# Performance work log

Measured on AMD Instinct MI355X. Metric: run time of the kernel, lower is better.

Reference implementation:

```python
import jax, jax.numpy as jnp
import numpy as np

B, T, U, D = 2, 512, 48, 512
H, K = 1024, 128  # hidden_channels, num_classes; fc1 in = 2*D = 1024


def setup_inputs() -> dict:
    key = jax.random.key(0)
    ks = jax.random.split(key, 9)
    s = 0.02
    return {
        "img_feature": jax.random.normal(ks[0], (B, T, D), jnp.float32),
        "label_feature": jax.random.normal(ks[1], (B, U, D), jnp.float32),
        "masks": jnp.ones((B, 1, T), jnp.float32),
        "W1": jax.random.normal(ks[2], (H, 2 * D), jnp.float32) * s,
        "b1": jnp.zeros((H,), jnp.float32),
        "W2": jax.random.normal(ks[3], (K, H), jnp.float32) * s,
        "b2": jnp.zeros((K,), jnp.float32),
        "conv_w": jax.random.normal(ks[4], (K, D), jnp.float32) * s,
        "conv_b": jnp.zeros((K,), jnp.float32),
    }


def reference(img_feature, label_feature, masks, W1, b1, W2, b2, conv_w, conv_b):
    # pointwise Conv1d over img features: (B,T,D) -> (B,K,T), masked
    img_seg_score = (jnp.einsum('btd,kd->bkt', img_feature, conv_w)
                     + conv_b[None, :, None]) * masks
    # fc1(cat(label, img)) == label @ Wl^T + img @ Wi^T + b1 (broadcast add),
    # avoiding the O(B*U*T*2D) repeat+cat intermediate.
    d = label_feature.shape[-1]
    Wl, Wi = W1[:, :d], W1[:, d:]
    lab = jnp.einsum('bud,hd->buh', label_feature, Wl)  # (B,U,H)
    img = jnp.einsum('btd,hd->bth', img_feature, Wi)    # (B,T,H)
    h = jnp.tanh(lab[:, :, None, :] + img[:, None, :, :] + b1)  # (B,U,T,H)
    joint = jnp.einsum('buth,kh->butk', h, W2) + b2
    joint_score = jax.nn.log_softmax(joint, axis=-1)
    return (img_seg_score, joint_score)
```

## Files before the change

### kernel.cpp

```cpp
#include <hip/hip_runtime.h>
#include <math.h>

#define BB 2
#define TT 512
#define UU 48
#define DD 512
#define HH 1024
#define KK 128

typedef _Float16 f16x8 __attribute__((ext_vector_type(8)));
typedef __fp16 fp16x2_t __attribute__((ext_vector_type(2)));
typedef float floatx4 __attribute__((ext_vector_type(4)));

__device__ __forceinline__ f16x8 tanh8z(f16x8 z) {
    f16x8 o;
#pragma unroll
    for (int i = 0; i < 8; i += 2) {
        float e0 = __builtin_amdgcn_exp2f((float)z[i]);
        float e1 = __builtin_amdgcn_exp2f((float)z[i + 1]);
        float r0 = __builtin_amdgcn_rcpf(e0 + 1.0f);
        float r1 = __builtin_amdgcn_rcpf(e1 + 1.0f);
        fp16x2_t p = __builtin_amdgcn_cvt_pkrtz(fmaf(-2.0f, r0, 1.0f),
                                                fmaf(-2.0f, r1, 1.0f));
        o[i] = (_Float16)p[0];
        o[i + 1] = (_Float16)p[1];
    }
    return o;
}

__global__ __launch_bounds__(256) void mid_kernel5(
    const float* __restrict__ img, const float* __restrict__ labf,
    const float* __restrict__ W1, const float* __restrict__ W2,
    const float* __restrict__ conv_w,
    const float* __restrict__ b1, const float* __restrict__ conv_b,
    const float* __restrict__ masks,
    _Float16* __restrict__ imgHf, _Float16* __restrict__ labHf,
    _Float16* __restrict__ W2s, float* __restrict__ seg_out) {
    int bid = blockIdx.x, tid = threadIdx.x;
    if (bid >= 624) {
        int base = (bid - 624) * 256 + tid;
#pragma unroll
        for (int i = 0; i < 32; ++i) {
            int o = base + i * 4096;
            int hg = o >> 10, kk2 = (o >> 3) & 127, hl = o & 7;
            W2s[o] = (_Float16)W2[(size_t)kk2 * HH + hg * 8 + hl];
        }
        return;
    }
    __shared__ __align__(16) _Float16 a_s[32][72];
    __shared__ __align__(16) _Float16 w_s[4096];
    const float* Arow;
    const float* Wbase;
    int r0, n0b, wstride, region;
    if (bid < 512) {
        region = 0; Arow = img; Wbase = W1 + 512; wstride = 2 * DD;
        int xcd = bid & 7, j = bid >> 3;
        r0 = (j & 31) * 32; n0b = (xcd * 2 + (j >> 5)) * 64;
    } else if (bid < 560) {
        region = 1; Arow = labf; Wbase = W1; wstride = 2 * DD;
        int i = bid - 512; r0 = (i % 3) * 32; n0b = (i / 3) * 64;
    } else {
        region = 2; Arow = img; Wbase = conv_w; wstride = DD;
        int i = bid - 560; r0 = (i >> 1) * 32; n0b = (i & 1) * 64;
    }
    int lane = tid & 63, wv = tid >> 6;
    int m0 = (wv & 1) * 16, n0w = (wv >> 1) * 32;
    int q = lane >> 4, r = lane & 15;
    int arow = tid >> 3, acol = (tid & 7) * 8;
    int wn = tid >> 2, wk0 = (tid & 3) * 16;
    const float* aptr = &Arow[(size_t)(r0 + arow) * DD + acol];
    const float* wptr = &Wbase[(size_t)(n0b + wn) * wstride + wk0];
    floatx4 acc[2] = {};
    float4 pa0, pa1, pw[4];
    pa0 = *(const float4*)aptr;
    pa1 = *(const float4*)(aptr + 4);
#pragma unroll
    for (int i2 = 0; i2 < 4; ++i2) pw[i2] = *(const float4*)(wptr + i2 * 4);
    for (int c = 0; c < 8; ++c) {
        f16x8 av;
        av[0] = (_Float16)pa0.x; av[1] = (_Float16)pa0.y;
        av[2] = (_Float16)pa0.z; av[3] = (_Float16)pa0.w;
        av[4] = (_Float16)pa1.x; av[5] = (_Float16)pa1.y;
        av[6] = (_Float16)pa1.z; av[7] = (_Float16)pa1.w;
        *(f16x8*)&a_s[arow][acol] = av;
        f16x8 w0, w1;
        w0[0] = (_Float16)pw[0].x; w0[1] = (_Float16)pw[0].y;
        w0[2] = (_Float16)pw[0].z; w0[3] = (_Float16)pw[0].w;
        w0[4] = (_Float16)pw[1].x; w0[5] = (_Float16)pw[1].y;
        w0[6] = (_Float16)pw[1].z; w0[7] = (_Float16)pw[1].w;
        w1[0] = (_Float16)pw[2].x; w1[1] = (_Float16)pw[2].y;
        w1[2] = (_Float16)pw[2].z; w1[3] = (_Float16)pw[2].w;
        w1[4] = (_Float16)pw[3].x; w1[5] = (_Float16)pw[3].y;
        w1[6] = (_Float16)pw[3].z; w1[7] = (_Float16)pw[3].w;
        int kg = wk0 >> 3;
        *(f16x8*)&w_s[((kg + 0) * 64 + wn) * 8] = w0;
        *(f16x8*)&w_s[((kg + 1) * 64 + wn) * 8] = w1;
        __syncthreads();
        if (c < 7) {
            int cb = (c + 1) * 64;
            pa0 = *(const float4*)(aptr + cb);
            pa1 = *(const float4*)(aptr + cb + 4);
#pragma unroll
            for (int i2 = 0; i2 < 4; ++i2)
                pw[i2] = *(const float4*)(wptr + cb + i2 * 4);
        }
#pragma unroll
        for (int kt = 0; kt < 2; ++kt) {
            f16x8 af = *(const f16x8*)&a_s[m0 + r][kt * 32 + q * 8];
#pragma unroll
            for (int nt = 0; nt < 2; ++nt) {
                f16x8 bf = *(const f16x8*)
                    &w_s[((kt * 4 + q) * 64 + n0w + nt * 16 + r) * 8];
                acc[nt] = __builtin_amdgcn_mfma_f32_16x16x32_f16(
                    af, bf, acc[nt], 0, 0, 0);
            }
        }
        __syncthreads();
    }
    const float SC = 2.8853900817779268f;
    if (region == 0) {
#pragma unroll
        for (int nt = 0; nt < 2; ++nt) {
            int n = n0b + n0w + nt * 16 + r;
#pragma unroll
            for (int rr = 0; rr < 4; ++rr)
                imgHf[(size_t)(r0 + m0 + 4 * q + rr) * HH + n] =
                    (_Float16)(acc[nt][rr] * SC);
        }
    } else if (region == 1) {
#pragma unroll
        for (int nt = 0; nt < 2; ++nt) {
            int n = n0b + n0w + nt * 16 + r;
            float bv = b1[n];
#pragma unroll
            for (int rr = 0; rr < 4; ++rr)
                labHf[(size_t)(r0 + m0 + 4 * q + rr) * HH + n] =
                    (_Float16)((acc[nt][rr] + bv) * SC);
        }
    } else {
#pragma unroll
        for (int nt = 0; nt < 2; ++nt) {
            int k = n0b + n0w + nt * 16 + r;
            float bv = conv_b[k];
#pragma unroll
            for (int rr = 0; rr < 4; ++rr) {
                int row = r0 + m0 + 4 * q + rr;
                int b = row >> 9, t = row & 511;
                seg_out[((size_t)b * KK + k) * TT + t] =
                    (acc[nt][rr] + bv) * masks[row];
            }
        }
    }
}

__global__ __launch_bounds__(192, 2) void joint_kernel7(
    const _Float16* __restrict__ imgHf,
    const _Float16* __restrict__ labHf,
    const _Float16* __restrict__ W2s,
    const float* __restrict__ b2,
    float* __restrict__ out) {
    __shared__ __align__(16) _Float16 w_s[2][8192];
    int tid = threadIdx.x, bid = blockIdx.x;
    int lane = tid & 63, wv = tid >> 6;
    int q = lane >> 4, r = lane & 15;
    int g0 = bid * 96 + wv * 32;
    int gr0 = g0 + r, gr1 = g0 + 16 + r;
    int bu0 = gr0 >> 9, t0 = gr0 & 511;
    int bu1 = gr1 >> 9, t1 = gr1 & 511;
    const _Float16* ir0 = imgHf + (size_t)(((bu0 >= UU) ? TT : 0) + t0) * HH;
    const _Float16* ir1 = imgHf + (size_t)(((bu1 >= UU) ? TT : 0) + t1) * HH;
    const _Float16* lr0 = labHf + (size_t)bu0 * HH;
    const _Float16* lr1 = labHf + (size_t)bu1 * HH;
    int c0 = q * 8, c1 = 32 + q * 8;
    floatx4 acc0[8] = {}, acc1[8] = {};
#pragma unroll
    for (int j = 0; j < 5; ++j)
        *(f16x8*)&w_s[0][(tid + j * 192) * 8] =
            *(const f16x8*)&W2s[(tid + j * 192) * 8];
    if (tid < 64)
        *(f16x8*)&w_s[0][(tid + 960) * 8] = *(const f16x8*)&W2s[(tid + 960) * 8];
    f16x8 i0A = *(const f16x8*)&ir0[c0], i0B = *(const f16x8*)&ir0[c1];
    f16x8 i1A = *(const f16x8*)&ir1[c0], i1B = *(const f16x8*)&ir1[c1];
    f16x8 l0A = *(const f16x8*)&lr0[c0], l0B = *(const f16x8*)&lr0[c1];
    f16x8 l1A = *(const f16x8*)&lr1[c0], l1B = *(const f16x8*)&lr1[c1];
    __syncthreads();
    for (int c = 0; c < 16; ++c) {
        _Float16* wb = w_s[c & 1];
        f16x8 ni0A, ni0B, ni1A, ni1B, nl0A, nl0B, nl1A, nl1B;
        f16x8 nw0, nw1, nw2, nw3, nw4, nw5;
        if (c < 15) {
            int cb = (c + 1) * 64;
            ni0A = *(const f16x8*)&ir0[cb + c0];
            ni0B = *(const f16x8*)&ir0[cb + c1];
            ni1A = *(const f16x8*)&ir1[cb + c0];
            ni1B = *(const f16x8*)&ir1[cb + c1];
            nl0A = *(const f16x8*)&lr0[cb + c0];
            nl0B = *(const f16x8*)&lr0[cb + c1];
            nl1A = *(const f16x8*)&lr1[cb + c0];
            nl1B = *(const f16x8*)&lr1[cb + c1];
            const _Float16* wsrc = W2s + (size_t)(c + 1) * 8192;
            nw0 = *(const f16x8*)&wsrc[(tid + 0 * 192) * 8];
            nw1 = *(const f16x8*)&wsrc[(tid + 1 * 192) * 8];
            nw2 = *(const f16x8*)&wsrc[(tid + 2 * 192) * 8];
            nw3 = *(const f16x8*)&wsrc[(tid + 3 * 192) * 8];
            nw4 = *(const f16x8*)&wsrc[(tid + 4 * 192) * 8];
            if (tid < 64) nw5 = *(const f16x8*)&wsrc[(tid + 960) * 8];
        }
        f16x8 a0A = tanh8z(i0A + l0A);
        f16x8 a1A = tanh8z(i1A + l1A);
#pragma unroll
        for (int nt = 0; nt < 8; ++nt) {
            f16x8 bf = *(const f16x8*)&wb[(q * 128 + nt * 16 + r) * 8];
            acc0[nt] = __builtin_amdgcn_mfma_f32_16x16x32_f16(
                a0A, bf, acc0[nt], 0, 0, 0);
            acc1[nt] = __builtin_amdgcn_mfma_f32_16x16x32_f16(
                a1A, bf, acc1[nt], 0, 0, 0);
        }
        f16x8 a0B = tanh8z(i0B + l0B);
        f16x8 a1B = tanh8z(i1B + l1B);
#pragma unroll
        for (int nt = 0; nt < 8; ++nt) {
            f16x8 bf = *(const f16x8*)&wb[((4 + q) * 128 + nt * 16 + r) * 8];
            acc0[nt] = __builtin_amdgcn_mfma_f32_16x16x32_f16(
                a0B, bf, acc0[nt], 0, 0, 0);
            acc1[nt] = __builtin_amdgcn_mfma_f32_16x16x32_f16(
                a1B, bf, acc1[nt], 0, 0, 0);
        }
        if (c < 15) {
            _Float16* wn_ = w_s[(c & 1) ^ 1];
            *(f16x8*)&wn_[(tid + 0 * 192) * 8] = nw0;
            *(f16x8*)&wn_[(tid + 1 * 192) * 8] = nw1;
            *(f16x8*)&wn_[(tid + 2 * 192) * 8] = nw2;
            *(f16x8*)&wn_[(tid + 3 * 192) * 8] = nw3;
            *(f16x8*)&wn_[(tid + 4 * 192) * 8] = nw4;
            if (tid < 64) *(f16x8*)&wn_[(tid + 960) * 8] = nw5;
            i0A = ni0A; i0B = ni0B; i1A = ni1A; i1B = ni1B;
            l0A = nl0A; l0B = nl0B; l1A = nl1A; l1B = nl1B;
        }
        __syncthreads();
    }
    float b2v[8];
#pragma unroll
    for (int nt = 0; nt < 8; ++nt) b2v[nt] = b2[nt * 16 + r];
#pragma unroll
    for (int mt = 0; mt < 2; ++mt) {
        float* obase = out + (size_t)(g0 + mt * 16 + 4 * q) * KK;
#pragma unroll
        for (int rr = 0; rr < 4; ++rr) {
            float v[8];
            float mx = -INFINITY;
#pragma unroll
            for (int nt = 0; nt < 8; ++nt) {
                v[nt] = (mt ? acc1[nt][rr] : acc0[nt][rr]) + b2v[nt];
                mx = fmaxf(mx, v[nt]);
            }
            mx = fmaxf(mx, __shfl_xor(mx, 1, 16));
            mx = fmaxf(mx, __shfl_xor(mx, 2, 16));
            mx = fmaxf(mx, __shfl_xor(mx, 4, 16));
            mx = fmaxf(mx, __shfl_xor(mx, 8, 16));
            float s = 0.f;
#pragma unroll
            for (int nt = 0; nt < 8; ++nt) s += __expf(v[nt] - mx);
            s += __shfl_xor(s, 1, 16);
            s += __shfl_xor(s, 2, 16);
            s += __shfl_xor(s, 4, 16);
            s += __shfl_xor(s, 8, 16);
            float lse = mx + __logf(s);
#pragma unroll
            for (int nt = 0; nt < 8; ++nt)
                obase[(size_t)rr * KK + nt * 16 + r] = v[nt] - lse;
        }
    }
}

extern "C" void kernel_launch(void* const* d_in, const int* in_sizes, int n_in,
                              void* d_out, int out_size, void* d_ws, size_t ws_size,
                              hipStream_t stream) {
    const float* img    = (const float*)d_in[0];
    const float* labf   = (const float*)d_in[1];
    const float* masks  = (const float*)d_in[2];
    const float* W1     = (const float*)d_in[3];
    const float* b1     = (const float*)d_in[4];
    const float* W2     = (const float*)d_in[5];
    const float* b2     = (const float*)d_in[6];
    const float* conv_w = (const float*)d_in[7];
    const float* conv_b = (const float*)d_in[8];
    float* out = (float*)d_out;

    _Float16* base  = (_Float16*)d_ws;
    _Float16* imgHf = base;
    _Float16* labHf = imgHf + 1024 * 1024;
    _Float16* W2s   = labHf + 96 * 1024;

    mid_kernel5<<<640, 256, 0, stream>>>(img, labf, W1, W2, conv_w,
                                         b1, conv_b, masks,
                                         imgHf, labHf, W2s, out);
    joint_kernel7<<<512, 192, 0, stream>>>(imgHf, labHf, W2s, b2,
                                           out + (size_t)BB * KK * TT);
}
```

Measured before the change: 125.9 us.

## Split joint kernel H reduction across two wave groups with LDS reduction

The joint kernel now uses 384 threads per block: two groups of three waves each handle half of the hidden dimension (8 chunks instead of 16) for the same 96 output rows. Each group keeps its own double-buffered W2 slice in shared memory, which grows shared memory to four buffers. Partial accumulators are exchanged through LDS and summed, and each group then computes log-softmax for one of the two 16-row tiles. The aim is to halve the serial loop length per wave and raise the number of waves in flight, at the cost of more shared memory, an extra reduction pass and possibly lower block occupancy.

```diff
diff --git a/kernel.cpp b/kernel.cpp
--- a/kernel.cpp
+++ b/kernel.cpp
@@ -153,43 +153,52 @@
     }
 }
 
-__global__ __launch_bounds__(192, 2) void joint_kernel7(
+__global__ __launch_bounds__(384, 3) void joint_kernel8(
     const _Float16* __restrict__ imgHf,
     const _Float16* __restrict__ labHf,
     const _Float16* __restrict__ W2s,
     const float* __restrict__ b2,
     float* __restrict__ out) {
-    __shared__ __align__(16) _Float16 w_s[2][8192];
+    __shared__ __align__(16) _Float16 w_s[4][8192];
     int tid = threadIdx.x, bid = blockIdx.x;
-    int lane = tid & 63, wv = tid >> 6;
+    int wv = tid >> 6;
+    int grp = (wv >= 3) ? 1 : 0;
+    int p = grp ? wv - 3 : wv;
+    int lt = tid - grp * 192;
+    int lane = tid & 63;
     int q = lane >> 4, r = lane & 15;
-    int g0 = bid * 96 + wv * 32;
+    int g0 = bid * 96 + p * 32;
     int gr0 = g0 + r, gr1 = g0 + 16 + r;
     int bu0 = gr0 >> 9, t0 = gr0 & 511;
     int bu1 = gr1 >> 9, t1 = gr1 & 511;
-    const _Float16* ir0 = imgHf + (size_t)(((bu0 >= UU) ? TT : 0) + t0) * HH;
-    const _Float16* ir1 = imgHf + (size_t)(((bu1 >= UU) ? TT : 0) + t1) * HH;
-    const _Float16* lr0 = labHf + (size_t)bu0 * HH;
-    const _Float16* lr1 = labHf + (size_t)bu1 * HH;
+    const _Float16* ir0 =
+        imgHf + (size_t)(((bu0 >= UU) ? TT : 0) + t0) * HH + grp * 512;
+    const _Float16* ir1 =
+        imgHf + (size_t)(((bu1 >= UU) ? TT : 0) + t1) * HH + grp * 512;
+    const _Float16* lr0 = labHf + (size_t)bu0 * HH + grp * 512;
+    const _Float16* lr1 = labHf + (size_t)bu1 * HH + grp * 512;
+    const _Float16* wsrc0 = W2s + (size_t)grp * 8 * 8192;
     int c0 = q * 8, c1 = 32 + q * 8;
     floatx4 acc0[8] = {}, acc1[8] = {};
+    _Float16* wbuf0 = w_s[grp * 2 + 0];
+    _Float16* wbuf1 = w_s[grp * 2 + 1];
 #pragma unroll
     for (int j = 0; j < 5; ++j)
-        *(f16x8*)&w_s[0][(tid + j * 192) * 8] =
-            *(const f16x8*)&W2s[(tid + j * 192) * 8];
-    if (tid < 64)
-        *(f16x8*)&w_s[0][(tid + 960) * 8] = *(const f16x8*)&W2s[(tid + 960) * 8];
+        *(f16x8*)&wbuf0[(lt + j * 192) * 8] =
+            *(const f16x8*)&wsrc0[(lt + j * 192) * 8];
+    if (lt < 64)
+        *(f16x8*)&wbuf0[(lt + 960) * 8] = *(const f16x8*)&wsrc0[(lt + 960) * 8];
     f16x8 i0A = *(const f16x8*)&ir0[c0], i0B = *(const f16x8*)&ir0[c1];
     f16x8 i1A = *(const f16x8*)&ir1[c0], i1B = *(const f16x8*)&ir1[c1];
     f16x8 l0A = *(const f16x8*)&lr0[c0], l0B = *(const f16x8*)&lr0[c1];
     f16x8 l1A = *(const f16x8*)&lr1[c0], l1B = *(const f16x8*)&lr1[c1];
     __syncthreads();
-    for (int c = 0; c < 16; ++c) {
-        _Float16* wb = w_s[c & 1];
+    for (int s = 0; s < 8; ++s) {
+        _Float16* wb = (s & 1) ? wbuf1 : wbuf0;
         f16x8 ni0A, ni0B, ni1A, ni1B, nl0A, nl0B, nl1A, nl1B;
         f16x8 nw0, nw1, nw2, nw3, nw4, nw5;
-        if (c < 15) {
-            int cb = (c + 1) * 64;
+        if (s < 7) {
+            int cb = (s + 1) * 64;
             ni0A = *(const f16x8*)&ir0[cb + c0];
             ni0B = *(const f16x8*)&ir0[cb + c1];
             ni1A = *(const f16x8*)&ir1[cb + c0];
@@ -198,13 +207,13 @@
             nl0B = *(const f16x8*)&lr0[cb + c1];
             nl1A = *(const f16x8*)&lr1[cb + c0];
             nl1B = *(const f16x8*)&lr1[cb + c1];
-            const _Float16* wsrc = W2s + (size_t)(c + 1) * 8192;
-            nw0 = *(const f16x8*)&wsrc[(tid + 0 * 192) * 8];
-            nw1 = *(const f16x8*)&wsrc[(tid + 1 * 192) * 8];
-            nw2 = *(const f16x8*)&wsrc[(tid + 2 * 192) * 8];
-            nw3 = *(const f16x8*)&wsrc[(tid + 3 * 192) * 8];
-            nw4 = *(const f16x8*)&wsrc[(tid + 4 * 192) * 8];
-            if (tid < 64) nw5 = *(const f16x8*)&wsrc[(tid + 960) * 8];
+            const _Float16* wsrc = wsrc0 + (size_t)(s + 1) * 8192;
+            nw0 = *(const f16x8*)&wsrc[(lt + 0 * 192) * 8];
+            nw1 = *(const f16x8*)&wsrc[(lt + 1 * 192) * 8];
+            nw2 = *(const f16x8*)&wsrc[(lt + 2 * 192) * 8];
+            nw3 = *(const f16x8*)&wsrc[(lt + 3 * 192) * 8];
+            nw4 = *(const f16x8*)&wsrc[(lt + 4 * 192) * 8];
+            if (lt < 64) nw5 = *(const f16x8*)&wsrc[(lt + 960) * 8];
         }
         f16x8 a0A = tanh8z(i0A + l0A);
         f16x8 a1A = tanh8z(i1A + l1A);
@@ -226,50 +235,63 @@
             acc1[nt] = __builtin_amdgcn_mfma_f32_16x16x32_f16(
                 a1B, bf, acc1[nt], 0, 0, 0);
         }
-        if (c < 15) {
-            _Float16* wn_ = w_s[(c & 1) ^ 1];
-            *(f16x8*)&wn_[(tid + 0 * 192) * 8] = nw0;
-            *(f16x8*)&wn_[(tid + 1 * 192) * 8] = nw1;
-            *(f16x8*)&wn_[(tid + 2 * 192) * 8] = nw2;
-            *(f16x8*)&wn_[(tid + 3 * 192) * 8] = nw3;
-            *(f16x8*)&wn_[(tid + 4 * 192) * 8] = nw4;
-            if (tid < 64) *(f16x8*)&wn_[(tid + 960) * 8] = nw5;
+        if (s < 7) {
+            _Float16* wn_ = (s & 1) ? wbuf0 : wbuf1;
+            *(f16x8*)&wn_[(lt + 0 * 192) * 8] = nw0;
+            *(f16x8*)&wn_[(lt + 1 * 192) * 8] = nw1;
+            *(f16x8*)&wn_[(lt + 2 * 192) * 8] = nw2;
+            *(f16x8*)&wn_[(lt + 3 * 192) * 8] = nw3;
+            *(f16x8*)&wn_[(lt + 4 * 192) * 8] = nw4;
+            if (lt < 64) *(f16x8*)&wn_[(lt + 960) * 8] = nw5;
             i0A = ni0A; i0B = ni0B; i1A = ni1A; i1B = ni1B;
             l0A = nl0A; l0B = nl0B; l1A = nl1A; l1B = nl1B;
         }
         __syncthreads();
     }
+    float* red = (float*)w_s;
+    {
+        float* myout = red + (size_t)(p * 2 + grp) * 2048;
+#pragma unroll
+        for (int nt = 0; nt < 8; ++nt)
+            *(floatx4*)&myout[nt * 256 + lane * 4] = grp ? acc0[nt] : acc1[nt];
+    }
+    __syncthreads();
+    {
+        float* other = red + (size_t)(p * 2 + (grp ^ 1)) * 2048;
+#pragma unroll
+        for (int nt = 0; nt < 8; ++nt) {
+            floatx4 v = *(const floatx4*)&other[nt * 256 + lane * 4];
+            if (grp) acc1[nt] += v; else acc0[nt] += v;
+        }
+    }
     float b2v[8];
 #pragma unroll
     for (int nt = 0; nt < 8; ++nt) b2v[nt] = b2[nt * 16 + r];
-#pragma unroll
-    for (int mt = 0; mt < 2; ++mt) {
-        float* obase = out + (size_t)(g0 + mt * 16 + 4 * q) * KK;
-#pragma unroll
-        for (int rr = 0; rr < 4; ++rr) {
-            float v[8];
-            float mx = -INFINITY;
-#pragma unroll
-            for (int nt = 0; nt < 8; ++nt) {
-                v[nt] = (mt ? acc1[nt][rr] : acc0[nt][rr]) + b2v[nt];
-                mx = fmaxf(mx, v[nt]);
-            }
-            mx = fmaxf(mx, __shfl_xor(mx, 1, 16));
-            mx = fmaxf(mx, __shfl_xor(mx, 2, 16));
-            mx = fmaxf(mx, __shfl_xor(mx, 4, 16));
-            mx = fmaxf(mx, __shfl_xor(mx, 8, 16));
-            float s = 0.f;
-#pragma unroll
-            for (int nt = 0; nt < 8; ++nt) s += __expf(v[nt] - mx);
-            s += __shfl_xor(s, 1, 16);
-            s += __shfl_xor(s, 2, 16);
-            s += __shfl_xor(s, 4, 16);
-            s += __shfl_xor(s, 8, 16);
-            float lse = mx + __logf(s);
-#pragma unroll
-            for (int nt = 0; nt < 8; ++nt)
-                obase[(size_t)rr * KK + nt * 16 + r] = v[nt] - lse;
-        }
+    float* obase = out + (size_t)(g0 + grp * 16 + 4 * q) * KK;
+#pragma unroll
+    for (int rr = 0; rr < 4; ++rr) {
+        float v[8];
+        float mx = -INFINITY;
+#pragma unroll
+        for (int nt = 0; nt < 8; ++nt) {
+            v[nt] = (grp ? acc1[nt][rr] : acc0[nt][rr]) + b2v[nt];
+            mx = fmaxf(mx, v[nt]);
+        }
+        mx = fmaxf(mx, __shfl_xor(mx, 1, 16));
+        mx = fmaxf(mx, __shfl_xor(mx, 2, 16));
+        mx = fmaxf(mx, __shfl_xor(mx, 4, 16));
+        mx = fmaxf(mx, __shfl_xor(mx, 8, 16));
+        float s = 0.f;
+#pragma unroll
+        for (int nt = 0; nt < 8; ++nt) s += __expf(v[nt] - mx);
+        s += __shfl_xor(s, 1, 16);
+        s += __shfl_xor(s, 2, 16);
+        s += __shfl_xor(s, 4, 16);
+        s += __shfl_xor(s, 8, 16);
+        float lse = mx + __logf(s);
+#pragma unroll
+        for (int nt = 0; nt < 8; ++nt)
+            obase[(size_t)rr * KK + nt * 16 + r] = v[nt] - lse;
     }
 }
 
@@ -295,6 +317,6 @@
     mid_kernel5<<<640, 256, 0, stream>>>(img, labf, W1, W2, conv_w,
                                          b1, conv_b, masks,
                                          imgHf, labHf, W2s, out);
-    joint_kernel7<<<512, 192, 0, stream>>>(imgHf, labHf, W2s, b2,
+    joint_kernel8<<<512, 384, 0, stream>>>(imgHf, labHf, W2s, b2,
                                            out + (size_t)BB * KK * TT);
 }
```

After: 128.7 us. +2.2%, slower.

## Use larger joint blocks with 4-chunk W2 staging per barrier

Applied to the files above, without the earlier changes.

Doubles the joint kernel block to 6 waves (192 rows) and launches half as many blocks. Each shared-memory W2 stage now holds four 64-wide H chunks (64 KB per buffer, 128 KB double-buffered), so barriers drop from 16 to 3 per block and each W2 load is shared by more rows. The costs are higher LDS usage, which may limit occupancy to one block per CU despite the launch bound of 2, more registers for the staged W2 prefetch, and only 256 blocks in the grid.

```diff
diff --git a/kernel.cpp b/kernel.cpp
--- a/kernel.cpp
+++ b/kernel.cpp
@@ -153,17 +153,17 @@
     }
 }
 
-__global__ __launch_bounds__(192, 2) void joint_kernel7(
+__global__ __launch_bounds__(384, 2) void joint_kernel9(
     const _Float16* __restrict__ imgHf,
     const _Float16* __restrict__ labHf,
     const _Float16* __restrict__ W2s,
     const float* __restrict__ b2,
     float* __restrict__ out) {
-    __shared__ __align__(16) _Float16 w_s[2][8192];
+    __shared__ __align__(16) _Float16 w_s[2][32768];
     int tid = threadIdx.x, bid = blockIdx.x;
     int lane = tid & 63, wv = tid >> 6;
-    int q = lane >> 4, r = lane & 15;
-    int g0 = bid * 96 + wv * 32;
+    int ql = lane >> 4, r = lane & 15;
+    int g0 = bid * 192 + wv * 32;
     int gr0 = g0 + r, gr1 = g0 + 16 + r;
     int bu0 = gr0 >> 9, t0 = gr0 & 511;
     int bu1 = gr1 >> 9, t1 = gr1 & 511;
@@ -171,80 +171,89 @@
     const _Float16* ir1 = imgHf + (size_t)(((bu1 >= UU) ? TT : 0) + t1) * HH;
     const _Float16* lr0 = labHf + (size_t)bu0 * HH;
     const _Float16* lr1 = labHf + (size_t)bu1 * HH;
-    int c0 = q * 8, c1 = 32 + q * 8;
+    int c0 = ql * 8, c1 = 32 + ql * 8;
     floatx4 acc0[8] = {}, acc1[8] = {};
 #pragma unroll
-    for (int j = 0; j < 5; ++j)
-        *(f16x8*)&w_s[0][(tid + j * 192) * 8] =
-            *(const f16x8*)&W2s[(tid + j * 192) * 8];
-    if (tid < 64)
-        *(f16x8*)&w_s[0][(tid + 960) * 8] = *(const f16x8*)&W2s[(tid + 960) * 8];
+    for (int k2 = 0; k2 < 10; ++k2)
+        *(f16x8*)&w_s[0][(tid + k2 * 384) * 8] =
+            *(const f16x8*)&W2s[(tid + k2 * 384) * 8];
+    if (tid < 256)
+        *(f16x8*)&w_s[0][(tid + 3840) * 8] =
+            *(const f16x8*)&W2s[(tid + 3840) * 8];
     f16x8 i0A = *(const f16x8*)&ir0[c0], i0B = *(const f16x8*)&ir0[c1];
     f16x8 i1A = *(const f16x8*)&ir1[c0], i1B = *(const f16x8*)&ir1[c1];
     f16x8 l0A = *(const f16x8*)&lr0[c0], l0B = *(const f16x8*)&lr0[c1];
     f16x8 l1A = *(const f16x8*)&lr1[c0], l1B = *(const f16x8*)&lr1[c1];
     __syncthreads();
-    for (int c = 0; c < 16; ++c) {
-        _Float16* wb = w_s[c & 1];
-        f16x8 ni0A, ni0B, ni1A, ni1B, nl0A, nl0B, nl1A, nl1B;
-        f16x8 nw0, nw1, nw2, nw3, nw4, nw5;
-        if (c < 15) {
-            int cb = (c + 1) * 64;
-            ni0A = *(const f16x8*)&ir0[cb + c0];
-            ni0B = *(const f16x8*)&ir0[cb + c1];
-            ni1A = *(const f16x8*)&ir1[cb + c0];
-            ni1B = *(const f16x8*)&ir1[cb + c1];
-            nl0A = *(const f16x8*)&lr0[cb + c0];
-            nl0B = *(const f16x8*)&lr0[cb + c1];
-            nl1A = *(const f16x8*)&lr1[cb + c0];
-            nl1B = *(const f16x8*)&lr1[cb + c1];
-            const _Float16* wsrc = W2s + (size_t)(c + 1) * 8192;
-            nw0 = *(const f16x8*)&wsrc[(tid + 0 * 192) * 8];
-            nw1 = *(const f16x8*)&wsrc[(tid + 1 * 192) * 8];
-            nw2 = *(const f16x8*)&wsrc[(tid + 2 * 192) * 8];
-            nw3 = *(const f16x8*)&wsrc[(tid + 3 * 192) * 8];
-            nw4 = *(const f16x8*)&wsrc[(tid + 4 * 192) * 8];
-            if (tid < 64) nw5 = *(const f16x8*)&wsrc[(tid + 960) * 8];
-        }
-        f16x8 a0A = tanh8z(i0A + l0A);
-        f16x8 a1A = tanh8z(i1A + l1A);
-#pragma unroll
-        for (int nt = 0; nt < 8; ++nt) {
-            f16x8 bf = *(const f16x8*)&wb[(q * 128 + nt * 16 + r) * 8];
-            acc0[nt] = __builtin_amdgcn_mfma_f32_16x16x32_f16(
-                a0A, bf, acc0[nt], 0, 0, 0);
-            acc1[nt] = __builtin_amdgcn_mfma_f32_16x16x32_f16(
-                a1A, bf, acc1[nt], 0, 0, 0);
-        }
-        f16x8 a0B = tanh8z(i0B + l0B);
-        f16x8 a1B = tanh8z(i1B + l1B);
-#pragma unroll
-        for (int nt = 0; nt < 8; ++nt) {
-            f16x8 bf = *(const f16x8*)&wb[((4 + q) * 128 + nt * 16 + r) * 8];
-            acc0[nt] = __builtin_amdgcn_mfma_f32_16x16x32_f16(
-                a0B, bf, acc0[nt], 0, 0, 0);
-            acc1[nt] = __builtin_amdgcn_mfma_f32_16x16x32_f16(
-                a1B, bf, acc1[nt], 0, 0, 0);
-        }
-        if (c < 15) {
-            _Float16* wn_ = w_s[(c & 1) ^ 1];
-            *(f16x8*)&wn_[(tid + 0 * 192) * 8] = nw0;
-            *(f16x8*)&wn_[(tid + 1 * 192) * 8] = nw1;
-            *(f16x8*)&wn_[(tid + 2 * 192) * 8] = nw2;
-            *(f16x8*)&wn_[(tid + 3 * 192) * 8] = nw3;
-            *(f16x8*)&wn_[(tid + 4 * 192) * 8] = nw4;
-            if (tid < 64) *(f16x8*)&wn_[(tid + 960) * 8] = nw5;
-            i0A = ni0A; i0B = ni0B; i1A = ni1A; i1B = ni1B;
-            l0A = nl0A; l0B = nl0B; l1A = nl1A; l1B = nl1B;
-        }
-        __syncthreads();
+    int buf = 0;
+    for (int qq = 0; qq < 4; ++qq) {
+        f16x8 wr[11];
+        if (qq < 3) {
+            const _Float16* wsrc = W2s + (size_t)(qq + 1) * 32768;
+#pragma unroll
+            for (int k2 = 0; k2 < 10; ++k2)
+                wr[k2] = *(const f16x8*)&wsrc[(tid + k2 * 384) * 8];
+            if (tid < 256) wr[10] = *(const f16x8*)&wsrc[(tid + 3840) * 8];
+        }
+        const _Float16* wb = w_s[buf];
+#pragma unroll
+        for (int c = 0; c < 4; ++c) {
+            int cc = qq * 4 + c;
+            f16x8 ni0A, ni0B, ni1A, ni1B, nl0A, nl0B, nl1A, nl1B;
+            if (cc < 15) {
+                int cb = (cc + 1) * 64;
+                ni0A = *(const f16x8*)&ir0[cb + c0];
+                ni0B = *(const f16x8*)&ir0[cb + c1];
+                ni1A = *(const f16x8*)&ir1[cb + c0];
+                ni1B = *(const f16x8*)&ir1[cb + c1];
+                nl0A = *(const f16x8*)&lr0[cb + c0];
+                nl0B = *(const f16x8*)&lr0[cb + c1];
+                nl1A = *(const f16x8*)&lr1[cb + c0];
+                nl1B = *(const f16x8*)&lr1[cb + c1];
+            }
+            f16x8 a0A = tanh8z(i0A + l0A);
+            f16x8 a1A = tanh8z(i1A + l1A);
+#pragma unroll
+            for (int nt = 0; nt < 8; ++nt) {
+                f16x8 bf = *(const f16x8*)
+                    &wb[c * 8192 + (ql * 128 + nt * 16 + r) * 8];
+                acc0[nt] = __builtin_amdgcn_mfma_f32_16x16x32_f16(
+                    a0A, bf, acc0[nt], 0, 0, 0);
+                acc1[nt] = __builtin_amdgcn_mfma_f32_16x16x32_f16(
+                    a1A, bf, acc1[nt], 0, 0, 0);
+            }
+            f16x8 a0B = tanh8z(i0B + l0B);
+            f16x8 a1B = tanh8z(i1B + l1B);
+#pragma unroll
+            for (int nt = 0; nt < 8; ++nt) {
+                f16x8 bf = *(const f16x8*)
+                    &wb[c * 8192 + ((4 + ql) * 128 + nt * 16 + r) * 8];
+                acc0[nt] = __builtin_amdgcn_mfma_f32_16x16x32_f16(
+                    a0B, bf, acc0[nt], 0, 0, 0);
+                acc1[nt] = __builtin_amdgcn_mfma_f32_16x16x32_f16(
+                    a1B, bf, acc1[nt], 0, 0, 0);
+            }
+            if (cc < 15) {
+                i0A = ni0A; i0B = ni0B; i1A = ni1A; i1B = ni1B;
+                l0A = nl0A; l0B = nl0B; l1A = nl1A; l1B = nl1B;
+            }
+        }
+        if (qq < 3) {
+            _Float16* wd = w_s[buf ^ 1];
+#pragma unroll
+            for (int k2 = 0; k2 < 10; ++k2)
+                *(f16x8*)&wd[(tid + k2 * 384) * 8] = wr[k2];
+            if (tid < 256) *(f16x8*)&wd[(tid + 3840) * 8] = wr[10];
+            __syncthreads();
+            buf ^= 1;
+        }
     }
     float b2v[8];
 #pragma unroll
     for (int nt = 0; nt < 8; ++nt) b2v[nt] = b2[nt * 16 + r];
 #pragma unroll
     for (int mt = 0; mt < 2; ++mt) {
-        float* obase = out + (size_t)(g0 + mt * 16 + 4 * q) * KK;
+        float* obase = out + (size_t)(g0 + mt * 16 + 4 * ql) * KK;
 #pragma unroll
         for (int rr = 0; rr < 4; ++rr) {
             float v[8];
@@ -295,6 +304,6 @@
     mid_kernel5<<<640, 256, 0, stream>>>(img, labf, W1, W2, conv_w,
                                          b1, conv_b, masks,
                                          imgHf, labHf, W2s, out);
-    joint_kernel7<<<512, 192, 0, stream>>>(imgHf, labHf, W2s, b2,
+    joint_kernel9<<<256, 384, 0, stream>>>(imgHf, labHf, W2s, b2,
                                            out + (size_t)BB * KK * TT);
 }
```

After: 124.5 us. No clear change (-1.1%).

## Stage joint kernel operands via async global_load_lds double buffering

Applied to the files above, without the earlier changes.

Replaces the register-staged prefetch of W2, image and label hidden rows with direct global-to-LDS asynchronous loads (global_load_lds) into double-buffered shared arrays. Label rows are loaded once per block into LDS and selected per row, instead of each thread reloading them. This cuts VGPR pressure and the explicit LDS store instructions. The cost is extra LDS usage per block and a dropped min-blocks launch bound, which may reduce occupancy.

```diff
diff --git a/kernel.cpp b/kernel.cpp
--- a/kernel.cpp
+++ b/kernel.cpp
@@ -11,6 +11,9 @@
 typedef _Float16 f16x8 __attribute__((ext_vector_type(8)));
 typedef __fp16 fp16x2_t __attribute__((ext_vector_type(2)));
 typedef float floatx4 __attribute__((ext_vector_type(4)));
+typedef __attribute__((address_space(3))) _Float16 lds_f16;
+typedef __attribute__((address_space(1))) const void g_cvoid;
+typedef __attribute__((address_space(3))) void l_void;
 
 __device__ __forceinline__ f16x8 tanh8z(f16x8 z) {
     f16x8 o;
@@ -153,64 +156,83 @@
     }
 }
 
-__global__ __launch_bounds__(192, 2) void joint_kernel7(
+__global__ __launch_bounds__(192) void joint_kernel11(
     const _Float16* __restrict__ imgHf,
     const _Float16* __restrict__ labHf,
     const _Float16* __restrict__ W2s,
     const float* __restrict__ b2,
     float* __restrict__ out) {
-    __shared__ __align__(16) _Float16 w_s[2][8192];
+    __shared__ __align__(16) _Float16 A_s[2][6144];
+    __shared__ __align__(16) _Float16 W_s[2][8192];
+    __shared__ __align__(16) _Float16 L_s[2][128];
     int tid = threadIdx.x, bid = blockIdx.x;
     int lane = tid & 63, wv = tid >> 6;
-    int q = lane >> 4, r = lane & 15;
+    int ql = lane >> 4, r = lane & 15;
     int g0 = bid * 96 + wv * 32;
-    int gr0 = g0 + r, gr1 = g0 + 16 + r;
-    int bu0 = gr0 >> 9, t0 = gr0 & 511;
-    int bu1 = gr1 >> 9, t1 = gr1 & 511;
-    const _Float16* ir0 = imgHf + (size_t)(((bu0 >= UU) ? TT : 0) + t0) * HH;
-    const _Float16* ir1 = imgHf + (size_t)(((bu1 >= UU) ? TT : 0) + t1) * HH;
-    const _Float16* lr0 = labHf + (size_t)bu0 * HH;
-    const _Float16* lr1 = labHf + (size_t)bu1 * HH;
-    int c0 = q * 8, c1 = 32 + q * 8;
+    int buA = (bid * 96) >> 9, buB = (bid * 96 + 95) >> 9;
+    int bu0 = (g0 + r) >> 9, bu1 = (g0 + 16 + r) >> 9;
+    int sel0 = (bu0 == buA) ? 0 : 64;
+    int sel1 = (bu1 == buA) ? 0 : 64;
     floatx4 acc0[8] = {}, acc1[8] = {};
-#pragma unroll
-    for (int j = 0; j < 5; ++j)
-        *(f16x8*)&w_s[0][(tid + j * 192) * 8] =
-            *(const f16x8*)&W2s[(tid + j * 192) * 8];
-    if (tid < 64)
-        *(f16x8*)&w_s[0][(tid + 960) * 8] = *(const f16x8*)&W2s[(tid + 960) * 8];
-    f16x8 i0A = *(const f16x8*)&ir0[c0], i0B = *(const f16x8*)&ir0[c1];
-    f16x8 i1A = *(const f16x8*)&ir1[c0], i1B = *(const f16x8*)&ir1[c1];
-    f16x8 l0A = *(const f16x8*)&lr0[c0], l0B = *(const f16x8*)&lr0[c1];
-    f16x8 l1A = *(const f16x8*)&lr1[c0], l1B = *(const f16x8*)&lr1[c1];
-    __syncthreads();
+
+    auto stage = [&](int cb, int buf) {
+        int cc = lane >> 4;
+#pragma unroll
+        for (int mh = 0; mh < 4; ++mh) {
+            int fl = g0 + (mh >> 1) * 16 + r;
+            int irow = ((fl >= UU * TT) ? TT : 0) + (fl & 511);
+            const _Float16* src =
+                imgHf + (size_t)irow * HH + cb + (mh & 1) * 32 + cc * 8;
+            lds_f16* dst = (lds_f16*)&A_s[buf][(wv * 4 + mh) * 512 + lane * 8];
+            __builtin_amdgcn_global_load_lds((g_cvoid*)src, (l_void*)dst,
+                                             16, 0, 0);
+        }
+        int i0 = wv * 5, nW = (wv == 2) ? 6 : 5;
+#pragma unroll
+        for (int j = 0; j < 6; ++j) {
+            if (j < nW) {
+                const _Float16* src =
+                    W2s + (size_t)cb * 128 + (i0 + j) * 512 + lane * 8;
+                lds_f16* dst =
+                    (lds_f16*)&W_s[buf][(i0 + j) * 512 + lane * 8];
+                __builtin_amdgcn_global_load_lds((g_cvoid*)src, (l_void*)dst,
+                                                 16, 0, 0);
+            }
+        }
+        if (wv == 0 && lane < 16) {
+            int bu = (lane < 8) ? buA : buB;
+            const _Float16* src = labHf + (size_t)bu * HH + cb + (lane & 7) * 8;
+            lds_f16* dst = (lds_f16*)&L_s[buf][lane * 8];
+            __builtin_amdgcn_global_load_lds((g_cvoid*)src, (l_void*)dst,
+                                             16, 0, 0);
+        }
+    };
+
+    stage(0, 0);
+    asm volatile("s_waitcnt vmcnt(0)" ::: "memory");
+    __builtin_amdgcn_s_barrier();
+    asm volatile("" ::: "memory");
+
+#pragma unroll 2
     for (int c = 0; c < 16; ++c) {
-        _Float16* wb = w_s[c & 1];
-        f16x8 ni0A, ni0B, ni1A, ni1B, nl0A, nl0B, nl1A, nl1B;
-        f16x8 nw0, nw1, nw2, nw3, nw4, nw5;
-        if (c < 15) {
-            int cb = (c + 1) * 64;
-            ni0A = *(const f16x8*)&ir0[cb + c0];
-            ni0B = *(const f16x8*)&ir0[cb + c1];
-            ni1A = *(const f16x8*)&ir1[cb + c0];
-            ni1B = *(const f16x8*)&ir1[cb + c1];
-            nl0A = *(const f16x8*)&lr0[cb + c0];
-            nl0B = *(const f16x8*)&lr0[cb + c1];
-            nl1A = *(const f16x8*)&lr1[cb + c0];
-            nl1B = *(const f16x8*)&lr1[cb + c1];
-            const _Float16* wsrc = W2s + (size_t)(c + 1) * 8192;
-            nw0 = *(const f16x8*)&wsrc[(tid + 0 * 192) * 8];
-            nw1 = *(const f16x8*)&wsrc[(tid + 1 * 192) * 8];
-            nw2 = *(const f16x8*)&wsrc[(tid + 2 * 192) * 8];
-            nw3 = *(const f16x8*)&wsrc[(tid + 3 * 192) * 8];
-            nw4 = *(const f16x8*)&wsrc[(tid + 4 * 192) * 8];
-            if (tid < 64) nw5 = *(const f16x8*)&wsrc[(tid + 960) * 8];
-        }
+        int cur = c & 1;
+        if (c < 15) stage((c + 1) * 64, cur ^ 1);
+        const _Float16* Ab = &A_s[cur][wv * 2048];
+        const _Float16* Wb = W_s[cur];
+        const _Float16* Lb = L_s[cur];
+        f16x8 i0A = *(const f16x8*)&Ab[0 * 512 + ql * 128 + r * 8];
+        f16x8 i0B = *(const f16x8*)&Ab[1 * 512 + ql * 128 + r * 8];
+        f16x8 i1A = *(const f16x8*)&Ab[2 * 512 + ql * 128 + r * 8];
+        f16x8 i1B = *(const f16x8*)&Ab[3 * 512 + ql * 128 + r * 8];
+        f16x8 l0A = *(const f16x8*)&Lb[sel0 + ql * 8];
+        f16x8 l0B = *(const f16x8*)&Lb[sel0 + 32 + ql * 8];
+        f16x8 l1A = *(const f16x8*)&Lb[sel1 + ql * 8];
+        f16x8 l1B = *(const f16x8*)&Lb[sel1 + 32 + ql * 8];
         f16x8 a0A = tanh8z(i0A + l0A);
         f16x8 a1A = tanh8z(i1A + l1A);
 #pragma unroll
         for (int nt = 0; nt < 8; ++nt) {
-            f16x8 bf = *(const f16x8*)&wb[(q * 128 + nt * 16 + r) * 8];
+            f16x8 bf = *(const f16x8*)&Wb[(ql * 128 + nt * 16 + r) * 8];
             acc0[nt] = __builtin_amdgcn_mfma_f32_16x16x32_f16(
                 a0A, bf, acc0[nt], 0, 0, 0);
             acc1[nt] = __builtin_amdgcn_mfma_f32_16x16x32_f16(
@@ -220,31 +242,24 @@
         f16x8 a1B = tanh8z(i1B + l1B);
 #pragma unroll
         for (int nt = 0; nt < 8; ++nt) {
-            f16x8 bf = *(const f16x8*)&wb[((4 + q) * 128 + nt * 16 + r) * 8];
+            f16x8 bf = *(const f16x8*)&Wb[((4 + ql) * 128 + nt * 16 + r) * 8];
             acc0[nt] = __builtin_amdgcn_mfma_f32_16x16x32_f16(
                 a0B, bf, acc0[nt], 0, 0, 0);
             acc1[nt] = __builtin_amdgcn_mfma_f32_16x16x32_f16(
                 a1B, bf, acc1[nt], 0, 0, 0);
         }
         if (c < 15) {
-            _Float16* wn_ = w_s[(c & 1) ^ 1];
-            *(f16x8*)&wn_[(tid + 0 * 192) * 8] = nw0;
-            *(f16x8*)&wn_[(tid + 1 * 192) * 8] = nw1;
-            *(f16x8*)&wn_[(tid + 2 * 192) * 8] = nw2;
-            *(f16x8*)&wn_[(tid + 3 * 192) * 8] = nw3;
-            *(f16x8*)&wn_[(tid + 4 * 192) * 8] = nw4;
-            if (tid < 64) *(f16x8*)&wn_[(tid + 960) * 8] = nw5;
-            i0A = ni0A; i0B = ni0B; i1A = ni1A; i1B = ni1B;
-            l0A = nl0A; l0B = nl0B; l1A = nl1A; l1B = nl1B;
-        }
-        __syncthreads();
+            asm volatile("s_waitcnt vmcnt(0)" ::: "memory");
+            __builtin_amdgcn_s_barrier();
+            asm volatile("" ::: "memory");
+        }
     }
     float b2v[8];
 #pragma unroll
     for (int nt = 0; nt < 8; ++nt) b2v[nt] = b2[nt * 16 + r];
 #pragma unroll
     for (int mt = 0; mt < 2; ++mt) {
-        float* obase = out + (size_t)(g0 + mt * 16 + 4 * q) * KK;
+        float* obase = out + (size_t)(g0 + mt * 16 + 4 * ql) * KK;
 #pragma unroll
         for (int rr = 0; rr < 4; ++rr) {
             float v[8];
@@ -295,6 +310,6 @@
     mid_kernel5<<<640, 256, 0, stream>>>(img, labf, W1, W2, conv_w,
                                          b1, conv_b, masks,
                                          imgHf, labHf, W2s, out);
-    joint_kernel7<<<512, 192, 0, stream>>>(imgHf, labHf, W2s, b2,
-                                           out + (size_t)BB * KK * TT);
+    joint_kernel11<<<512, 192, 0, stream>>>(imgHf, labHf, W2s, b2,
+                                            out + (size_t)BB * KK * TT);
 }
```

Result: no change. 124.3 us (-1.3%).
